# Kernel optimization log

Measured on AMD Instinct MI355X. Metric: run time of the kernel, lower is better.

Reference implementation:

```python
import jax, jax.numpy as jnp
import numpy as np

N, K, IN_DIM, OUT_DIM = 100000, 16, 64, 64
BN_EPS = 1e-5


def setup_inputs() -> dict:
    key = jax.random.key(0)
    ks = jax.random.split(key, 12)
    def lin(k, fan_in, shape):
        bound = 1.0 / np.sqrt(fan_in)
        return jax.random.uniform(k, shape, jnp.float32, -bound, bound)
    return {
        'points': jax.random.normal(ks[0], (N, 3), jnp.float32),
        'neighbors': jax.random.randint(ks[1], (N, K), 0, N + 1, jnp.int32),
        'feats': jax.random.normal(ks[2], (N, IN_DIM), jnp.float32),
        'q_w': lin(ks[3], IN_DIM, (OUT_DIM, IN_DIM)), 'q_b': lin(ks[3], IN_DIM, (OUT_DIM,)),
        'k_w': lin(ks[4], IN_DIM, (OUT_DIM, IN_DIM)), 'k_b': lin(ks[4], IN_DIM, (OUT_DIM,)),
        'v_w': lin(ks[5], IN_DIM, (OUT_DIM, IN_DIM)), 'v_b': lin(ks[5], IN_DIM, (OUT_DIM,)),
        'p_w': lin(ks[6], 3, (OUT_DIM, 3)), 'p_b': lin(ks[6], 3, (OUT_DIM,)),
        'p_gamma': jnp.ones((OUT_DIM,), jnp.float32), 'p_beta': jnp.zeros((OUT_DIM,), jnp.float32),
        'w_w': lin(ks[7], OUT_DIM, (OUT_DIM, OUT_DIM)), 'w_b': lin(ks[7], OUT_DIM, (OUT_DIM,)),
        'w_gamma': jnp.ones((OUT_DIM,), jnp.float32), 'w_beta': jnp.zeros((OUT_DIM,), jnp.float32),
    }


def _bn_relu(x, gamma, beta):
    # BatchNorm1d (training mode, biased var) over all axes except channel (last), then ReLU
    mean = jnp.mean(x, axis=(0, 1), keepdims=True)
    var = jnp.mean(jnp.square(x - mean), axis=(0, 1), keepdims=True)
    y = (x - mean) * jax.lax.rsqrt(var + BN_EPS) * gamma + beta
    return jax.nn.relu(y)


def reference(points, neighbors, feats, q_w, q_b, k_w, k_b, v_w, v_b,
              p_w, p_b, p_gamma, p_beta, w_w, w_b, w_gamma, w_beta):
    q = feats @ q_w.T + q_b                       # [N, D]
    k = feats @ k_w.T + k_b
    v = feats @ v_w.T + v_b
    # shadow-pad with an out-of-range point / zero feats
    points_pad = jnp.concatenate([points, jnp.full((1, 3), 1e6, points.dtype)], 0)
    k_pad = jnp.concatenate([k, jnp.zeros((1, k.shape[1]), k.dtype)], 0)
    v_pad = jnp.concatenate([v, jnp.zeros((1, v.shape[1]), v.dtype)], 0)
    p_g = points_pad[neighbors]                   # [N, K, 3]
    k_g = k_pad[neighbors]                        # [N, K, D]
    v_g = v_pad[neighbors]                        # [N, K, D]
    p_feats = _bn_relu(p_g @ p_w.T + p_b, p_gamma, p_beta)          # [N, K, D]
    w = k_g * q[:, None, :] + p_feats                               # [N, K, D]
    w = _bn_relu(w @ w_w.T + w_b, w_gamma, w_beta)
    w = jax.nn.softmax(w, axis=1)                 # softmax over neighbor axis
    att = jnp.sum((v_g + p_feats) * w, axis=1)    # [N, D]
    return att
```

## Files before the change

### kernel.cpp

```cpp
#include <hip/hip_runtime.h>
#include <math.h>

#define NP 100000
#define KN 16
#define DIM 64
constexpr float BN_EPS_F = 1e-5f;
constexpr double MS = (double)NP * (double)KN;

typedef __attribute__((ext_vector_type(8))) short short8;
typedef __attribute__((ext_vector_type(4))) float f32x4;

constexpr size_t B_S1  = 0;
constexpr size_t B_PWE = 128;
constexpr size_t B_S2  = 1152;
constexpr size_t B_BN2 = 2176;
constexpr size_t B_ZSE = 2688;
constexpr size_t B_ZSB = 2944;
constexpr size_t B_PFS = 3200;
constexpr size_t B_PTS = 4096;
constexpr size_t B_Q   = 1204224;
constexpr size_t B_U   = B_Q + (size_t)NP * DIM * 2;
constexpr size_t B_KK  = B_U + (size_t)(NP + 1) * DIM * 2;
constexpr size_t B_Z1   = B_KK + (size_t)(NP + 1) * DIM * 4;
constexpr size_t B_END1 = B_Z1 + (size_t)NP * 2048;
constexpr size_t B_Z2   = B_KK + (size_t)(NP + 1) * DIM * 2;
constexpr size_t B_END2 = B_Z2 + (size_t)NP * 2048;

__device__ __forceinline__ ushort f2bf(float f) {
  union { float f; unsigned u; } v; v.f = f;
  unsigned u = v.u + 0x7fffu + ((v.u >> 16) & 1u);
  return (ushort)(u >> 16);
}
__device__ __forceinline__ float bf2f(ushort b) {
  union { unsigned u; float f; } v; v.u = ((unsigned)b) << 16;
  return v.f;
}
__device__ __forceinline__ float u2f(unsigned u) {
  union { unsigned u; float f; } v; v.u = u; return v.f;
}

__device__ __forceinline__ void load_wfrags(const float* __restrict__ ww, int lane,
                                            short8 wf[4][2]) {
  int co = lane & 15, g = lane >> 4;
#pragma unroll
  for (int tn = 0; tn < 4; ++tn)
#pragma unroll
    for (int kk = 0; kk < 2; ++kk) {
      const float* p = ww + (size_t)(co + 16 * tn) * DIM + kk * 32 + g * 8;
      short8 f;
#pragma unroll
      for (int j = 0; j < 8; ++j) f[j] = (short)f2bf(p[j]);
      wf[tn][kk] = f;
    }
}

__global__ void k_init(char* __restrict__ wsb) {
  int t = threadIdx.x;
  double* s1 = (double*)(wsb + B_S1);
  double* s2 = (double*)(wsb + B_S2);
  if (t < 10) s1[t] = 0.0;
  if (t < 128) s2[t] = 0.0;
  if (t < 32)
    ((unsigned*)(wsb + B_U))[(size_t)NP * 32 + t] = 0u;
}

__global__ __launch_bounds__(256) void k_pts(const float* __restrict__ pts,
                                             char* __restrict__ wsb) {
  int t = blockIdx.x * 256 + threadIdx.x;
  float* p3 = (float*)(wsb + B_PTS);
  if (t < NP * 3) p3[t] = pts[t];
  else if (t < NP * 3 + 3) p3[t] = 1e6f;
}

__global__ __launch_bounds__(256) void k_stats1(const int* __restrict__ nbr,
    char* __restrict__ wsb) {
  const float* p3 = (const float*)(wsb + B_PTS);
  double a[10] = {0, 0, 0, 0, 0, 0, 0, 0, 0, 0};
  int stride = gridDim.x * blockDim.x;
  for (int e = blockIdx.x * 256 + threadIdx.x; e < NP * KN; e += stride) {
    int idx = nbr[e];
    const float* pr = p3 + (size_t)idx * 3;
    float x = pr[0], y = pr[1], z = pr[2];
    a[9] += (idx >= NP) ? 1.0 : 0.0;
    a[0] += x; a[1] += y; a[2] += z;
    a[3] += (double)x * x; a[4] += (double)x * y; a[5] += (double)x * z;
    a[6] += (double)y * y; a[7] += (double)y * z; a[8] += (double)z * z;
  }
  __shared__ double red[256];
  double* s1 = (double*)(wsb + B_S1);
  for (int j = 0; j < 10; ++j) {
    red[threadIdx.x] = a[j];
    __syncthreads();
    for (int s = 128; s > 0; s >>= 1) {
      if (threadIdx.x < s) red[threadIdx.x] += red[threadIdx.x + s];
      __syncthreads();
    }
    if (threadIdx.x == 0) atomicAdd(&s1[j], red[0]);
    __syncthreads();
  }
}

__global__ void k_fold1(const float* __restrict__ pw, const float* __restrict__ pb,
                        const float* __restrict__ pg, const float* __restrict__ pbeta,
                        char* __restrict__ wsb) {
  int c = threadIdx.x;
  if (c >= DIM) return;
  double* s1 = (double*)(wsb + B_S1);
  double inv = 1.0 / MS;
  double m0 = s1[0] * inv, m1 = s1[1] * inv, m2 = s1[2] * inv;
  double C00 = s1[3] * inv - m0 * m0, C01 = s1[4] * inv - m0 * m1;
  double C02 = s1[5] * inv - m0 * m2, C11 = s1[6] * inv - m1 * m1;
  double C12 = s1[7] * inv - m1 * m2, C22 = s1[8] * inv - m2 * m2;
  double w0 = pw[c * 3], w1 = pw[c * 3 + 1], w2 = pw[c * 3 + 2];
  double mean = w0 * m0 + w1 * m1 + w2 * m2 + (double)pb[c];
  double var = w0 * w0 * C00 + w1 * w1 * C11 + w2 * w2 * C22
             + 2.0 * (w0 * w1 * C01 + w0 * w2 * C02 + w1 * w2 * C12);
  if (var < 0.0) var = 0.0;
  double a = (double)pg[c] / sqrt(var + (double)BN_EPS_F);
  float4 o;
  o.x = (float)(w0 * a); o.y = (float)(w1 * a); o.z = (float)(w2 * a);
  o.w = (float)(((double)pb[c] - mean) * a + (double)pbeta[c]);
  ((float4*)(wsb + B_PWE))[c] = o;
}

__global__ void k_shadow(const float* __restrict__ ww, const float* __restrict__ wb,
                         char* __restrict__ wsb, int kpmode) {
  __shared__ float pfs[64], pfb[64];
  int c = threadIdx.x;
  if (c >= DIM) return;
  float4 pwe = ((const float4*)(wsb + B_PWE))[c];
  float pf = fmaxf(fmaf(pwe.x, 1e6f, fmaf(pwe.y, 1e6f, fmaf(pwe.z, 1e6f, pwe.w))), 0.f);
  pfs[c] = pf;
  pfb[c] = bf2f(f2bf(pf));
  ((float*)(wsb + B_PFS))[c] = pf;
  if (kpmode)
    ((unsigned*)(wsb + B_KK))[(size_t)NP * DIM + c] = ((unsigned)f2bf(pf) << 16);
  else
    ((ushort*)(wsb + B_KK))[(size_t)NP * DIM + c] = 0;
  __syncthreads();
  double ze = (double)wb[c], zb = (double)wb[c];
  for (int i = 0; i < DIM; ++i) {
    float w = ww[c * DIM + i];
    ze += (double)pfs[i] * (double)w;
    zb += (double)pfb[i] * (double)bf2f(f2bf(w));
  }
  ((float*)(wsb + B_ZSE))[c] = (float)ze;
  ((float*)(wsb + B_ZSB))[c] = (float)zb;
}

template<bool KPMODE>
__global__ __launch_bounds__(256) void k_qkv(const float* __restrict__ feats,
    const float* __restrict__ qw, const float* __restrict__ qb,
    const float* __restrict__ kw, const float* __restrict__ kb,
    const float* __restrict__ vw, const float* __restrict__ vb,
    char* __restrict__ wsb) {
  __shared__ float wq[4096], wk[4096], wv[4096];
  int tid = threadIdx.x;
  for (int e = tid; e < 4096; e += 256) {
    int cc = e >> 6, i = e & 63;
    int d = (i >> 2) * 256 + cc * 4 + (i & 3);
    wq[d] = qw[e]; wk[d] = kw[e]; wv[d] = vw[e];
  }
  __syncthreads();
  int p = tid >> 6, c = tid & 63;
  float bq = qb[c], bk = kb[c], bv = vb[c];
  float4 pwe = ((const float4*)(wsb + B_PWE))[c];
  const float4* f4 = (const float4*)feats;
  const float* p3 = (const float*)(wsb + B_PTS);
  ushort* qt = (ushort*)(wsb + B_Q);
  ushort* ut = (ushort*)(wsb + B_U);
  int stride = gridDim.x * 4;
  for (int n = blockIdx.x * 4 + p; n < NP; n += stride) {
    float px = p3[(size_t)n * 3], py = p3[(size_t)n * 3 + 1], pz = p3[(size_t)n * 3 + 2];
    float aq = bq, ak = bk, av = bv;
#pragma unroll
    for (int i4 = 0; i4 < 16; ++i4) {
      float4 fv = f4[(size_t)n * 16 + i4];
      float4 a  = *(const float4*)(wq + i4 * 256 + c * 4);
      float4 b  = *(const float4*)(wk + i4 * 256 + c * 4);
      float4 g  = *(const float4*)(wv + i4 * 256 + c * 4);
      aq = fmaf(a.x, fv.x, aq); aq = fmaf(a.y, fv.y, aq);
      aq = fmaf(a.z, fv.z, aq); aq = fmaf(a.w, fv.w, aq);
      ak = fmaf(b.x, fv.x, ak); ak = fmaf(b.y, fv.y, ak);
      ak = fmaf(b.z, fv.z, ak); ak = fmaf(b.w, fv.w, ak);
      av = fmaf(g.x, fv.x, av); av = fmaf(g.y, fv.y, av);
      av = fmaf(g.z, fv.z, av); av = fmaf(g.w, fv.w, av);
    }
    float pf = fmaxf(fmaf(pwe.x, px, fmaf(pwe.y, py, fmaf(pwe.z, pz, pwe.w))), 0.f);
    qt[(size_t)n * DIM + c] = f2bf(aq);
    if (KPMODE)
      ((unsigned*)(wsb + B_KK))[(size_t)n * DIM + c] =
          ((unsigned)f2bf(pf) << 16) | (unsigned)f2bf(ak);
    else
      ((ushort*)(wsb + B_KK))[(size_t)n * DIM + c] = f2bf(ak);
    ut[(size_t)n * DIM + c] = f2bf(av + pf);
  }
}

#define LOADN(SET, nn) {                                                      \
  const int4* p4_ = (const int4*)(nbr + (size_t)(nn) * KN);                   \
  int4 b0_ = p4_[0], b1_ = p4_[1], b2_ = p4_[2], b3_ = p4_[3];                \
  i##SET[0] = b0_.x; i##SET[1] = b0_.y; i##SET[2] = b0_.z; i##SET[3] = b0_.w; \
  i##SET[4] = b1_.x; i##SET[5] = b1_.y; i##SET[6] = b1_.z; i##SET[7] = b1_.w; \
  i##SET[8] = b2_.x; i##SET[9] = b2_.y; i##SET[10]= b2_.z; i##SET[11]= b2_.w; \
  i##SET[12]= b3_.x; i##SET[13]= b3_.y; i##SET[14]= b3_.z; i##SET[15]= b3_.w; }

#define S2_LOADG(SET, nn) {                                                   \
  if constexpr (KPMODE) {                                                     \
    _Pragma("unroll") for (int k = 0; k < KN; ++k)                            \
      kp##SET[k] = kpt[(size_t)i##SET[k] * DIM + c];                          \
  } else {                                                                    \
    _Pragma("unroll") for (int k = 0; k < KN; ++k) {                          \
      int ik_ = i##SET[k];                                                    \
      unsigned kv_ = kt[(size_t)ik_ * DIM + c];                               \
      const float* pr_ = p3 + (size_t)ik_ * 3;                                \
      float px_ = pr_[0], py_ = pr_[1], pz_ = pr_[2];                         \
      float pf_ = fmaxf(fmaf(pwe.x, px_, fmaf(pwe.y, py_,                     \
                        fmaf(pwe.z, pz_, pwe.w))), 0.f);                      \
      kp##SET[k] = ((unsigned)f2bf(pf_) << 16) | kv_;                         \
    }                                                                         \
  }                                                                           \
  q##SET = bf2f(qt[(size_t)(nn) * DIM + c]); }

#define S2_COMPUTE(SET, nn) {                                                 \
  _Pragma("unroll") for (int k = 0; k < KN; ++k) {                            \
    float kg_ = u2f(kp##SET[k] << 16);                                        \
    float pf_ = u2f(kp##SET[k] & 0xffff0000u);                                \
    hw[k * 64 + (c ^ ((k & 7) << 3))] = f2bf(fmaf(kg_, q##SET, pf_));         \
  }                                                                           \
  __builtin_amdgcn_wave_barrier();                                            \
  short8 a0_ = *(short8*)&hw[aoff0];                                          \
  short8 a1_ = *(short8*)&hw[aoff1];                                          \
  char* zr_ = ztc + (size_t)(nn) * 2048 + g * 8;                              \
  _Pragma("unroll") for (int tn = 0; tn < 4; ++tn) {                          \
    f32x4 acc_ = {wbv[tn], wbv[tn], wbv[tn], wbv[tn]};                        \
    acc_ = __builtin_amdgcn_mfma_f32_16x16x32_bf16(a0_, wf[tn][0], acc_,0,0,0);\
    acc_ = __builtin_amdgcn_mfma_f32_16x16x32_bf16(a1_, wf[tn][1], acc_,0,0,0);\
    _Pragma("unroll") for (int r = 0; r < 4; ++r) {                           \
      float zv_ = acc_[r];                                                    \
      s[tn] += zv_; ssq[tn] = fmaf(zv_, zv_, ssq[tn]); }                      \
    uint2 w_;                                                                 \
    w_.x = (unsigned)f2bf(acc_[0]) | ((unsigned)f2bf(acc_[1]) << 16);         \
    w_.y = (unsigned)f2bf(acc_[2]) | ((unsigned)f2bf(acc_[3]) << 16);         \
    *(uint2*)(zr_ + ((lane & 15) + 16 * tn) * 32) = w_;                       \
  }                                                                           \
  __builtin_amdgcn_wave_barrier(); }

template<bool KPMODE>
__global__ __launch_bounds__(256) void k_stats2(const int* __restrict__ nbr,
    const float* __restrict__ ww, const float* __restrict__ wbias,
    char* __restrict__ wsb, char* __restrict__ ztc) {
  __shared__ ushort hl[4][16 * 64];
  __shared__ float sred[4][64], ssred[4][64];
  int tid = threadIdx.x, wid = tid >> 6, lane = tid & 63, c = lane;
  short8 wf[4][2];
  load_wfrags(ww, lane, wf);
  float wbv[4];
#pragma unroll
  for (int tn = 0; tn < 4; ++tn) wbv[tn] = wbias[(lane & 15) + 16 * tn];
  const ushort* qt = (const ushort*)(wsb + B_Q);
  const ushort* kt = (const ushort*)(wsb + B_KK);
  const unsigned* kpt = (const unsigned*)(wsb + B_KK);
  const float* p3 = (const float*)(wsb + B_PTS);
  float4 pwe = ((const float4*)(wsb + B_PWE))[c];
  ushort* hw = hl[wid];
  int row = lane & 15, g = lane >> 4;
  int aoff0 = row * 64 + ((g * 8) ^ ((row & 7) << 3));
  int aoff1 = row * 64 + ((32 + g * 8) ^ ((row & 7) << 3));
  float s[4] = {0, 0, 0, 0}, ssq[4] = {0, 0, 0, 0};
  const int S = gridDim.x * 4;
  int n = blockIdx.x * 4 + wid;

  int iA[KN], iB[KN];
  unsigned kpA[KN], kpB[KN];
  float qA, qB;

  LOADN(A, n)
  LOADN(B, n + S)
  S2_LOADG(A, n)
  for (int it = 0; it < 4; ++it) {
    S2_LOADG(B, n + S)
    if (it < 3) LOADN(A, n + 2 * S)
    S2_COMPUTE(A, n)
    if (it < 3) { S2_LOADG(A, n + 2 * S) LOADN(B, n + 3 * S) }
    S2_COMPUTE(B, n + S)
    n += 2 * S;
  }
#pragma unroll
  for (int t = 0; t < 4; ++t) {
    s[t] += __shfl_xor(s[t], 16);    s[t] += __shfl_xor(s[t], 32);
    ssq[t] += __shfl_xor(ssq[t], 16); ssq[t] += __shfl_xor(ssq[t], 32);
  }
  if (lane < 16) {
#pragma unroll
    for (int t = 0; t < 4; ++t) { sred[wid][lane + 16 * t] = s[t]; ssred[wid][lane + 16 * t] = ssq[t]; }
  }
  __syncthreads();
  if (tid < DIM) {
    double SS0 = 0.0, SS1 = 0.0;
    for (int w = 0; w < 4; ++w) { SS0 += (double)sred[w][tid]; SS1 += (double)ssred[w][tid]; }
    double* s2 = (double*)(wsb + B_S2);
    atomicAdd(&s2[tid], SS0);
    atomicAdd(&s2[DIM + tid], SS1);
  }
}

__global__ void k_fold2(const float* __restrict__ wg, const float* __restrict__ wbeta,
                        char* __restrict__ wsb) {
  int c = threadIdx.x;
  if (c >= DIM) return;
  double* s2 = (double*)(wsb + B_S2);
  double* s1 = (double*)(wsb + B_S1);
  double nsh = s1[9];
  double zse = (double)((float*)(wsb + B_ZSE))[c];
  double zsb = (double)((float*)(wsb + B_ZSB))[c];
  double S  = s2[c] + nsh * (zse - zsb);
  double SS = s2[DIM + c] + nsh * (zse * zse - zsb * zsb);
  double mean = S / MS;
  double var = SS / MS - mean * mean;
  if (var < 0.0) var = 0.0;
  double a = (double)wg[c] / sqrt(var + (double)BN_EPS_F);
  ((float*)(wsb + B_BN2))[c] = (float)a;
  ((float*)(wsb + B_BN2))[DIM + c] = (float)((double)wbeta[c] - mean * a);
}

#define FS_LOADG(SET, nn) {                                                   \
  const char* zr_ = ztc + (size_t)(nn) * 2048 + c * 32;                       \
  *(uint4*)&zz##SET[0] = *(const uint4*)(zr_);                                \
  *(uint4*)&zz##SET[4] = *(const uint4*)(zr_ + 16);                           \
  _Pragma("unroll") for (int k = 0; k < KN; ++k)                              \
    uv##SET[k] = ut[(size_t)i##SET[k] * DIM + c];                             \
  sh##SET = 0u;                                                               \
  _Pragma("unroll") for (int k = 0; k < KN; ++k)                              \
    sh##SET |= (unsigned)(i##SET[k] >= NP) << k; }

#define FS_COMPUTE(SET, nn) {                                                 \
  float lg_[KN];                                                              \
  float m_ = 0.f;                                                             \
  _Pragma("unroll") for (int k = 0; k < KN; ++k) {                            \
    float lin_ = bf2f((ushort)(zz##SET[k >> 1] >> ((k & 1) * 16)));           \
    if ((sh##SET >> k) & 1u) lin_ = zsec;                                     \
    float t_ = fmaxf(fmaf(lin_, fsc, fsh), 0.f);                              \
    lg_[k] = t_; m_ = fmaxf(m_, t_); }                                        \
  float se_ = 0.f;                                                            \
  _Pragma("unroll") for (int k = 0; k < KN; ++k) {                            \
    float e_ = __expf(lg_[k] - m_); lg_[k] = e_; se_ += e_; }                 \
  float rs_ = 1.0f / se_;                                                     \
  float att_ = 0.f;                                                           \
  _Pragma("unroll") for (int k = 0; k < KN; ++k) {                            \
    float u_ = ((sh##SET >> k) & 1u) ? pfsec : bf2f(uv##SET[k]);              \
    att_ = fmaf(u_, lg_[k] * rs_, att_); }                                    \
  out[(size_t)(nn) * DIM + c] = att_; }

__global__ __launch_bounds__(256) void k_final_str(const int* __restrict__ nbr,
    const char* __restrict__ wsb, const char* __restrict__ ztc,
    float* __restrict__ out) {
  int tid = threadIdx.x, wid = tid >> 6, c = tid & 63;
  const ushort* ut = (const ushort*)(wsb + B_U);
  const float* bn2 = (const float*)(wsb + B_BN2);
  float fsc = bn2[c], fsh = bn2[DIM + c];
  float zsec = ((const float*)(wsb + B_ZSE))[c];
  float pfsec = ((const float*)(wsb + B_PFS))[c];
  const int S = gridDim.x * 4;
  int n = blockIdx.x * 4 + wid;

  int iA[KN], iB[KN];
  unsigned zzA[8], zzB[8];
  ushort uvA[KN], uvB[KN];
  unsigned shA, shB;

  LOADN(A, n)
  LOADN(B, n + S)
  FS_LOADG(A, n)
  for (int it = 0; it < 4; ++it) {
    FS_LOADG(B, n + S)
    if (it < 3) LOADN(A, n + 2 * S)
    FS_COMPUTE(A, n)
    if (it < 3) { FS_LOADG(A, n + 2 * S) LOADN(B, n + 3 * S) }
    FS_COMPUTE(B, n + S)
    n += 2 * S;
  }
}

extern "C" void kernel_launch(void* const* d_in, const int* in_sizes, int n_in,
                              void* d_out, int out_size, void* d_ws, size_t ws_size,
                              hipStream_t stream) {
  const float* pts   = (const float*)d_in[0];
  const int*   nbr   = (const int*)d_in[1];
  const float* feats = (const float*)d_in[2];
  const float* qw = (const float*)d_in[3];  const float* qb = (const float*)d_in[4];
  const float* kw = (const float*)d_in[5];  const float* kb = (const float*)d_in[6];
  const float* vw = (const float*)d_in[7];  const float* vb = (const float*)d_in[8];
  const float* pw = (const float*)d_in[9];  const float* pb = (const float*)d_in[10];
  const float* pg = (const float*)d_in[11]; const float* pbeta = (const float*)d_in[12];
  const float* www = (const float*)d_in[13]; const float* wb = (const float*)d_in[14];
  const float* wg  = (const float*)d_in[15]; const float* wbeta = (const float*)d_in[16];
  char* wsb = (char*)d_ws;
  float* out = (float*)d_out;

  const bool kpmode = (ws_size >= B_END1);
  char* zt = wsb + (kpmode ? B_Z1 : B_Z2);

  hipLaunchKernelGGL(k_init,   dim3(1),    dim3(256), 0, stream, wsb);
  hipLaunchKernelGGL(k_pts,    dim3(1173), dim3(256), 0, stream, pts, wsb);
  hipLaunchKernelGGL(k_stats1, dim3(512),  dim3(256), 0, stream, nbr, wsb);
  hipLaunchKernelGGL(k_fold1,  dim3(1),    dim3(64),  0, stream, pw, pb, pg, pbeta, wsb);
  hipLaunchKernelGGL(k_shadow, dim3(1),    dim3(64),  0, stream, www, wb, wsb, (int)kpmode);
  if (kpmode) {
    hipLaunchKernelGGL((k_qkv<true>),    dim3(1024), dim3(256), 0, stream,
                       feats, qw, qb, kw, kb, vw, vb, wsb);
    hipLaunchKernelGGL((k_stats2<true>), dim3(3125), dim3(256), 0, stream,
                       nbr, www, wb, wsb, zt);
  } else {
    hipLaunchKernelGGL((k_qkv<false>),    dim3(1024), dim3(256), 0, stream,
                       feats, qw, qb, kw, kb, vw, vb, wsb);
    hipLaunchKernelGGL((k_stats2<false>), dim3(3125), dim3(256), 0, stream,
                       nbr, www, wb, wsb, zt);
  }
  hipLaunchKernelGGL(k_fold2, dim3(1), dim3(64), 0, stream, wg, wbeta, wsb);
  hipLaunchKernelGGL(k_final_str, dim3(3125), dim3(256), 0, stream, nbr, wsb, zt, out);
}
```

Before: 349.3 us.

## Compute QKV projection with bf16 MFMA tiles instead of scalar FMAs

Replaces the scalar-FMA QKV projection kernel, which staged fp32 weights in shared memory, with a wavefront-per-16-row-tile kernel. Each tile uses bf16 MFMA 16x16x32 instructions, with the weight fragments held in registers. This cuts ALU and LDS cost for the three 64x64 projections. In exchange, features are rounded to bf16 before the matmul rather than only the outputs, which reduces accuracy, and the stores are now strided per lane rather than coalesced. The grid drops from 1024 to 256 blocks.

After: 289.6 us. 17.1% less time.

```diff
diff --git a/kernel.cpp b/kernel.cpp
--- a/kernel.cpp
+++ b/kernel.cpp
@@ -52,6 +52,15 @@
       for (int j = 0; j < 8; ++j) f[j] = (short)f2bf(p[j]);
       wf[tn][kk] = f;
     }
+}
+
+__device__ __forceinline__ short8 pack_bf8(float4 a, float4 b) {
+  short8 r;
+  r[0] = (short)f2bf(a.x); r[1] = (short)f2bf(a.y);
+  r[2] = (short)f2bf(a.z); r[3] = (short)f2bf(a.w);
+  r[4] = (short)f2bf(b.x); r[5] = (short)f2bf(b.y);
+  r[6] = (short)f2bf(b.z); r[7] = (short)f2bf(b.w);
+  return r;
 }
 
 __global__ void k_init(char* __restrict__ wsb) {
@@ -149,51 +158,86 @@
 }
 
 template<bool KPMODE>
-__global__ __launch_bounds__(256) void k_qkv(const float* __restrict__ feats,
+__global__ __launch_bounds__(256, 2) void k_qkv_mfma(const float* __restrict__ feats,
     const float* __restrict__ qw, const float* __restrict__ qb,
     const float* __restrict__ kw, const float* __restrict__ kb,
     const float* __restrict__ vw, const float* __restrict__ vb,
     char* __restrict__ wsb) {
-  __shared__ float wq[4096], wk[4096], wv[4096];
-  int tid = threadIdx.x;
-  for (int e = tid; e < 4096; e += 256) {
-    int cc = e >> 6, i = e & 63;
-    int d = (i >> 2) * 256 + cc * 4 + (i & 3);
-    wq[d] = qw[e]; wk[d] = kw[e]; wv[d] = vw[e];
-  }
-  __syncthreads();
-  int p = tid >> 6, c = tid & 63;
-  float bq = qb[c], bk = kb[c], bv = vb[c];
-  float4 pwe = ((const float4*)(wsb + B_PWE))[c];
-  const float4* f4 = (const float4*)feats;
+  int tid = threadIdx.x, wid = tid >> 6, lane = tid & 63;
+  int co = lane & 15, g = lane >> 4;
+  short8 wfq[4][2], wfk[4][2], wfv[4][2];
+  load_wfrags(qw, lane, wfq);
+  load_wfrags(kw, lane, wfk);
+  load_wfrags(vw, lane, wfv);
+  float bq[4], bk[4], bv[4];
+  float4 pwe4[4];
+#pragma unroll
+  for (int tn = 0; tn < 4; ++tn) {
+    bq[tn] = qb[co + 16 * tn];
+    bk[tn] = kb[co + 16 * tn];
+    bv[tn] = vb[co + 16 * tn];
+    pwe4[tn] = ((const float4*)(wsb + B_PWE))[co + 16 * tn];
+  }
   const float* p3 = (const float*)(wsb + B_PTS);
   ushort* qt = (ushort*)(wsb + B_Q);
   ushort* ut = (ushort*)(wsb + B_U);
-  int stride = gridDim.x * 4;
-  for (int n = blockIdx.x * 4 + p; n < NP; n += stride) {
-    float px = p3[(size_t)n * 3], py = p3[(size_t)n * 3 + 1], pz = p3[(size_t)n * 3 + 2];
-    float aq = bq, ak = bk, av = bv;
-#pragma unroll
-    for (int i4 = 0; i4 < 16; ++i4) {
-      float4 fv = f4[(size_t)n * 16 + i4];
-      float4 a  = *(const float4*)(wq + i4 * 256 + c * 4);
-      float4 b  = *(const float4*)(wk + i4 * 256 + c * 4);
-      float4 g  = *(const float4*)(wv + i4 * 256 + c * 4);
-      aq = fmaf(a.x, fv.x, aq); aq = fmaf(a.y, fv.y, aq);
-      aq = fmaf(a.z, fv.z, aq); aq = fmaf(a.w, fv.w, aq);
-      ak = fmaf(b.x, fv.x, ak); ak = fmaf(b.y, fv.y, ak);
-      ak = fmaf(b.z, fv.z, ak); ak = fmaf(b.w, fv.w, ak);
-      av = fmaf(g.x, fv.x, av); av = fmaf(g.y, fv.y, av);
-      av = fmaf(g.z, fv.z, av); av = fmaf(g.w, fv.w, av);
-    }
-    float pf = fmaxf(fmaf(pwe.x, px, fmaf(pwe.y, py, fmaf(pwe.z, pz, pwe.w))), 0.f);
-    qt[(size_t)n * DIM + c] = f2bf(aq);
-    if (KPMODE)
-      ((unsigned*)(wsb + B_KK))[(size_t)n * DIM + c] =
-          ((unsigned)f2bf(pf) << 16) | (unsigned)f2bf(ak);
-    else
-      ((ushort*)(wsb + B_KK))[(size_t)n * DIM + c] = f2bf(ak);
-    ut[(size_t)n * DIM + c] = f2bf(av + pf);
+  ushort* kt = (ushort*)(wsb + B_KK);
+  unsigned* kpt = (unsigned*)(wsb + B_KK);
+  const int NT = NP / 16;
+  for (int t = blockIdx.x * 4 + wid; t < NT; t += gridDim.x * 4) {
+    const float* fr = feats + ((size_t)t * 16 + co) * DIM + g * 8;
+    float4 f0 = *(const float4*)fr;
+    float4 f1 = *(const float4*)(fr + 4);
+    float4 f2 = *(const float4*)(fr + 32);
+    float4 f3 = *(const float4*)(fr + 36);
+    short8 a0 = pack_bf8(f0, f1);
+    short8 a1 = pack_bf8(f2, f3);
+    int nb = t * 16 + g * 4;
+    float px[4], py[4], pz[4];
+#pragma unroll
+    for (int r = 0; r < 4; ++r) {
+      const float* pr = p3 + (size_t)(nb + r) * 3;
+      px[r] = pr[0]; py[r] = pr[1]; pz[r] = pr[2];
+    }
+    float pf[4][4];
+#pragma unroll
+    for (int tn = 0; tn < 4; ++tn)
+#pragma unroll
+      for (int r = 0; r < 4; ++r)
+        pf[tn][r] = fmaxf(fmaf(pwe4[tn].x, px[r], fmaf(pwe4[tn].y, py[r],
+                          fmaf(pwe4[tn].z, pz[r], pwe4[tn].w))), 0.f);
+#pragma unroll
+    for (int tn = 0; tn < 4; ++tn) {
+      f32x4 acc = {bq[tn], bq[tn], bq[tn], bq[tn]};
+      acc = __builtin_amdgcn_mfma_f32_16x16x32_bf16(a0, wfq[tn][0], acc, 0, 0, 0);
+      acc = __builtin_amdgcn_mfma_f32_16x16x32_bf16(a1, wfq[tn][1], acc, 0, 0, 0);
+#pragma unroll
+      for (int r = 0; r < 4; ++r)
+        qt[(size_t)(nb + r) * DIM + co + 16 * tn] = f2bf(acc[r]);
+    }
+#pragma unroll
+    for (int tn = 0; tn < 4; ++tn) {
+      f32x4 acc = {bk[tn], bk[tn], bk[tn], bk[tn]};
+      acc = __builtin_amdgcn_mfma_f32_16x16x32_bf16(a0, wfk[tn][0], acc, 0, 0, 0);
+      acc = __builtin_amdgcn_mfma_f32_16x16x32_bf16(a1, wfk[tn][1], acc, 0, 0, 0);
+#pragma unroll
+      for (int r = 0; r < 4; ++r) {
+        if (KPMODE)
+          kpt[(size_t)(nb + r) * DIM + co + 16 * tn] =
+              ((unsigned)f2bf(pf[tn][r]) << 16) | (unsigned)f2bf(acc[r]);
+        else
+          kt[(size_t)(nb + r) * DIM + co + 16 * tn] = f2bf(acc[r]);
+      }
+    }
+#pragma unroll
+    for (int tn = 0; tn < 4; ++tn) {
+      f32x4 acc = {bv[tn], bv[tn], bv[tn], bv[tn]};
+      acc = __builtin_amdgcn_mfma_f32_16x16x32_bf16(a0, wfv[tn][0], acc, 0, 0, 0);
+      acc = __builtin_amdgcn_mfma_f32_16x16x32_bf16(a1, wfv[tn][1], acc, 0, 0, 0);
+#pragma unroll
+      for (int r = 0; r < 4; ++r)
+        ut[(size_t)(nb + r) * DIM + co + 16 * tn] = f2bf(acc[r] + pf[tn][r]);
+    }
   }
 }
 
@@ -407,14 +451,14 @@
   hipLaunchKernelGGL(k_fold1,  dim3(1),    dim3(64),  0, stream, pw, pb, pg, pbeta, wsb);
   hipLaunchKernelGGL(k_shadow, dim3(1),    dim3(64),  0, stream, www, wb, wsb, (int)kpmode);
   if (kpmode) {
-    hipLaunchKernelGGL((k_qkv<true>),    dim3(1024), dim3(256), 0, stream,
+    hipLaunchKernelGGL((k_qkv_mfma<true>), dim3(256),  dim3(256), 0, stream,
                        feats, qw, qb, kw, kb, vw, vb, wsb);
-    hipLaunchKernelGGL((k_stats2<true>), dim3(3125), dim3(256), 0, stream,
+    hipLaunchKernelGGL((k_stats2<true>),   dim3(3125), dim3(256), 0, stream,
                        nbr, www, wb, wsb, zt);
   } else {
-    hipLaunchKernelGGL((k_qkv<false>),    dim3(1024), dim3(256), 0, stream,
+    hipLaunchKernelGGL((k_qkv_mfma<false>), dim3(256),  dim3(256), 0, stream,
                        feats, qw, qb, kw, kb, vw, vb, wsb);
-    hipLaunchKernelGGL((k_stats2<false>), dim3(3125), dim3(256), 0, stream,
+    hipLaunchKernelGGL((k_stats2<false>),   dim3(3125), dim3(256), 0, stream,
                        nbr, www, wb, wsb, zt);
   }
   hipLaunchKernelGGL(k_fold2, dim3(1), dim3(64), 0, stream, wg, wbeta, wsb);
```
